# Kernel optimization log

Measured on AMD Instinct MI355X. Metric: run time of the kernel, lower is better.

## Reference

```python
import jax, jax.numpy as jnp
import numpy as np

B = 8
INPUT_SHAPE = (32, 32, 32)
N = int(np.prod(INPUT_SHAPE))  # 32768
K = 128


def setup_inputs() -> dict:
    key = jax.random.key(0)
    k1, k2, k3, k4 = jax.random.split(key, 4)
    data = jax.random.normal(k1, (B,) + INPUT_SHAPE, dtype=jnp.float32)
    mask = jax.random.uniform(k2, (B,) + INPUT_SHAPE, dtype=jnp.float32)
    mult = jax.random.normal(k3, (N, K), dtype=jnp.float32) * 0.05  # RandomNormal init
    sigma_sq = jax.random.normal(k4, (1,), dtype=jnp.float32) * 0.05
    return {"data": data, "mask": mask, "mult": mult, "sigma_sq": sigma_sq}


def reference(data, mask, mult, sigma_sq):
    # Two-arg branch of SpatiallySparseDense_old.call (a_fact == 1).
    b = data.shape[0]
    n, k = mult.shape
    data_flat = data.reshape(b, n)          # [B, N]
    mask_flat = mask.reshape(b, n)          # [B, N]
    # W0 = mask_flat * mult, per batch: [B, N, K]
    W0 = mask_flat[:, :, None] * mult[None, :, :]
    # Gram matrix W0^T W0 + sigma^2 * I : [B, K, K]
    gram = jnp.einsum('bnk,bnl->bkl', W0, W0)
    seye = sigma_sq[0] * jnp.eye(k, dtype=data.dtype)
    pre = jnp.linalg.inv(gram + seye[None])  # [B, K, K] (matches tf.linalg.inv)
    # m = W0^T data : [B, K, 1]
    m = jnp.einsum('bnk,bn->bk', W0, data_flat)[..., None]
    res = jnp.matmul(pre, m)                # [B, K, 1]
    return res
```

## Files before the change

### kernel.cpp

```cpp
#include <hip/hip_runtime.h>

#define BATCH 8
#define NN 32768
#define KK 128
#define NCHUNK 32
#define CHUNK 1024
#define NST 16
#define NITER 12

typedef __attribute__((ext_vector_type(8)))  _Float16 half8;
typedef __attribute__((ext_vector_type(4)))  _Float16 half4;
typedef __attribute__((ext_vector_type(16))) float    f32x16;

#define MT_OFF   0ull
#define WH_OFF   (MT_OFF + 8388608ull)
#define DH_OFF   (WH_OFF + 524288ull)
#define GP_OFF   (DH_OFF + 524288ull)
#define MP_OFF   (GP_OFF + 5242880ull)
#define G_OFF    (MP_OFF + 131072ull)

__global__ __launch_bounds__(256) void conv_kernel(
    const float* __restrict__ data, const float* __restrict__ mask,
    unsigned char* __restrict__ ws)
{
    const int gid = blockIdx.x * 256 + threadIdx.x;
    const float4 d4 = ((const float4*)data)[gid];
    const float4 m4 = ((const float4*)mask)[gid];
    half4 w = { (_Float16)m4.x, (_Float16)m4.y, (_Float16)m4.z, (_Float16)m4.w };
    half4 d = { (_Float16)d4.x, (_Float16)d4.y, (_Float16)d4.z, (_Float16)d4.w };
    ((half4*)(ws + WH_OFF))[gid] = w;
    ((half4*)(ws + DH_OFF))[gid] = d;
}

__global__ __launch_bounds__(256) void transpose_kernel(
    const float* __restrict__ mult, unsigned char* __restrict__ ws)
{
    __shared__ _Float16 t[128][136];
    const int tid = threadIdx.x;
    const int n0  = blockIdx.x * 128;
    const float4* m4 = (const float4*)mult;
#pragma unroll
    for (int u = 0; u < 16; ++u) {
        const int c16 = u * 256 + tid;
        const int n  = c16 >> 5;
        const int kq = c16 & 31;
        float4 v = m4[(size_t)(n0 + n) * 32 + kq];
        half4 h = { (_Float16)v.x, (_Float16)v.y, (_Float16)v.z, (_Float16)v.w };
        *(half4*)&t[n][kq * 4] = h;
    }
    __syncthreads();
    _Float16* mt = (_Float16*)(ws + MT_OFF);
    const int k = tid & 127, nh = tid >> 7;
#pragma unroll
    for (int i = 0; i < 8; ++i) {
        const int nb = nh * 64 + i * 8;
        half8 v;
#pragma unroll
        for (int j = 0; j < 8; ++j) v[j] = t[nb + j][k];
        *(half8*)(mt + (size_t)k * NN + n0 + nb) = v;
    }
}

__global__ __launch_bounds__(256, 1) void gram_kernel(
    unsigned char* __restrict__ ws)
{
    __shared__ unsigned char smem[36864];
    const int tid = threadIdx.x;
    const int b     = blockIdx.x >> 5;
    const int chunk = blockIdx.x & 31;
    const int n0    = chunk * CHUNK;
    const int w = tid >> 6, l = tid & 63;

    const _Float16* mt = (const _Float16*)(ws + MT_OFF);

    if (tid < 128) {
        half8 wv = *(const half8*)((const _Float16*)(ws + WH_OFF) + (size_t)b * NN + n0 + tid * 8);
        half8 dv = *(const half8*)((const _Float16*)(ws + DH_OFF) + (size_t)b * NN + n0 + tid * 8);
        *(half8*)(smem + 32768 + tid * 16) = wv;
        *(half8*)(smem + 34816 + tid * 16) = dv;
    }

    const int krow = tid >> 3;
    const int gd   = tid & 7;
    const _Float16* gsrc0 = mt + (size_t)krow * NN + n0 + gd * 8;
    const int wslot = (gd ^ (krow & 7)) * 16;

    uint4 S0, S1, S2, S3;
#define GLOAD(st_) { const _Float16* p = gsrc0 + (size_t)(st_) * 64;          \
        S0 = *(const uint4*)(p);                                              \
        S1 = *(const uint4*)(p + (size_t)32 * NN);                            \
        S2 = *(const uint4*)(p + (size_t)64 * NN);                            \
        S3 = *(const uint4*)(p + (size_t)96 * NN); }
#define DSWRITE(buf_) { unsigned char* bp = smem + (buf_) * 16384 + krow * 128 + wslot; \
        *(uint4*)(bp)         = S0;  *(uint4*)(bp + 4096)  = S1;              \
        *(uint4*)(bp + 8192)  = S2;  *(uint4*)(bp + 12288) = S3; }

    const int frow  = (l & 31) * 128;
    const int fslot = ((w * 2 + (l >> 5)) ^ (l & 7)) * 16;
    const int wdoff = w * 32 + (l >> 5) * 16;

    f32x16 a00 = {}, a01 = {}, a02 = {}, a03 = {}, a11 = {},
           a12 = {}, a13 = {}, a22 = {}, a23 = {}, a33 = {};
    float macc0 = 0.f, macc1 = 0.f, macc2 = 0.f, macc3 = 0.f;

    GLOAD(0);
    __syncthreads();
    DSWRITE(0);
    GLOAD(1);
    __syncthreads();

#pragma unroll 2
    for (int st = 0; st < NST; ++st) {
        const int cur = st & 1;
        if (st < NST - 1) {
            DSWRITE(cur ^ 1);
            if (st < NST - 2) GLOAD(st + 2);
        }
        const unsigned char* tb = smem + cur * 16384;
        const half8 wf = *(const half8*)(smem + 32768 + st * 128 + wdoff);
        const half8 df = *(const half8*)(smem + 34816 + st * 128 + wdoff);
        half8 f0 = *(const half8*)(tb +     0 + frow + fslot) * wf;
        half8 f1 = *(const half8*)(tb +  4096 + frow + fslot) * wf;
        half8 f2 = *(const half8*)(tb +  8192 + frow + fslot) * wf;
        half8 f3 = *(const half8*)(tb + 12288 + frow + fslot) * wf;
#pragma unroll
        for (int j = 0; j < 8; ++j) {
            const float dj = (float)df[j];
            macc0 = fmaf((float)f0[j], dj, macc0);
            macc1 = fmaf((float)f1[j], dj, macc1);
            macc2 = fmaf((float)f2[j], dj, macc2);
            macc3 = fmaf((float)f3[j], dj, macc3);
        }
        a00 = __builtin_amdgcn_mfma_f32_32x32x16_f16(f0, f0, a00, 0, 0, 0);
        a01 = __builtin_amdgcn_mfma_f32_32x32x16_f16(f0, f1, a01, 0, 0, 0);
        a02 = __builtin_amdgcn_mfma_f32_32x32x16_f16(f0, f2, a02, 0, 0, 0);
        a03 = __builtin_amdgcn_mfma_f32_32x32x16_f16(f0, f3, a03, 0, 0, 0);
        a11 = __builtin_amdgcn_mfma_f32_32x32x16_f16(f1, f1, a11, 0, 0, 0);
        a12 = __builtin_amdgcn_mfma_f32_32x32x16_f16(f1, f2, a12, 0, 0, 0);
        a13 = __builtin_amdgcn_mfma_f32_32x32x16_f16(f1, f3, a13, 0, 0, 0);
        a22 = __builtin_amdgcn_mfma_f32_32x32x16_f16(f2, f2, a22, 0, 0, 0);
        a23 = __builtin_amdgcn_mfma_f32_32x32x16_f16(f2, f3, a23, 0, 0, 0);
        a33 = __builtin_amdgcn_mfma_f32_32x32x16_f16(f3, f3, a33, 0, 0, 0);
        __syncthreads();
    }

    {
        float* M = (float*)(smem + 32768);
        const int base = (w * 2 + (l >> 5)) * 128 + (l & 31);
        M[base +  0] = macc0;  M[base + 32] = macc1;
        M[base + 64] = macc2;  M[base + 96] = macc3;
    }
    _Float16* Gp = (_Float16*)(ws + GP_OFF) + (size_t)(b * NCHUNK + chunk) * 10240;
    float* Mp = (float*)(ws + MP_OFF) + (size_t)(b * NCHUNK + chunk) * KK;
    float* R = (float*)smem;

#define PHASE(p_, A0_, A1_)                                                    \
    {                                                                          \
        *(f32x16*)(R + (w * 2 + 0) * 1024 + l * 16) = A0_;                     \
        *(f32x16*)(R + (w * 2 + 1) * 1024 + l * 16) = A1_;                     \
        __syncthreads();                                                       \
        _Pragma("unroll")                                                      \
        for (int pass = 0; pass < 2; ++pass) {                                 \
            const int e = pass * 1024 + tid * 4;                               \
            float4 s0 = *(float4*)(R + e);                                     \
            float4 s1 = *(float4*)(R + 2048 + e);                              \
            float4 s2 = *(float4*)(R + 4096 + e);                              \
            float4 s3 = *(float4*)(R + 6144 + e);                              \
            float sx = s0.x + s1.x + s2.x + s3.x;                              \
            float sy = s0.y + s1.y + s2.y + s3.y;                              \
            float sz = s0.z + s1.z + s2.z + s3.z;                              \
            float sw = s0.w + s1.w + s2.w + s3.w;                              \
            half4 h = { (_Float16)sx, (_Float16)sy, (_Float16)sz, (_Float16)sw }; \
            *(half4*)(Gp + (p_) * 2048 + e) = h;                               \
        }                                                                      \
        if ((p_) == 0 && tid < 128) {                                          \
            const float* M = (const float*)(smem + 32768);                     \
            float s = 0.f;                                                     \
            _Pragma("unroll")                                                  \
            for (int c8 = 0; c8 < 8; ++c8) s += M[c8 * 128 + tid];             \
            Mp[tid] = s;                                                       \
        }                                                                      \
        __syncthreads();                                                       \
    }

    PHASE(0, a00, a01)
    PHASE(1, a02, a03)
    PHASE(2, a11, a12)
    PHASE(3, a13, a22)
    PHASE(4, a23, a33)
#undef PHASE
#undef GLOAD
#undef DSWRITE
}

__global__ __launch_bounds__(256) void reduce_kernel(
    const float* __restrict__ sig, unsigned char* __restrict__ ws)
{
    const int tid = threadIdx.x;
    const int b  = blockIdx.x >> 6;
    const int jb = blockIdx.x & 63;
    const int j  = jb * 256 + tid;
    const int r = j >> 7, c = j & 127;
    const int t = r >> 5, u = c >> 5;
    int tt, uu, rr, cc;
    if (t <= u) { tt = t; uu = u; rr = r & 31; cc = c & 31; }
    else        { tt = u; uu = t; rr = c & 31; cc = r & 31; }
    const int tidx = tt * 4 - tt * (tt + 1) / 2 + uu;
    const int lane = cc + 32 * ((rr >> 2) & 1);
    const int reg  = (rr & 3) + 4 * ((rr >> 3) & 3);
    const _Float16* Gp = (const _Float16*)(ws + GP_OFF)
                       + (size_t)b * NCHUNK * 10240
                       + (size_t)tidx * 1024 + lane * 16 + reg;
    float s = 0.f;
#pragma unroll
    for (int ch = 0; ch < NCHUNK; ++ch) s += (float)Gp[(size_t)ch * 10240];
    if (r == c) s += sig[0];
    ((float*)(ws + G_OFF))[(size_t)b * 16384 + j] = s;
}

__device__ __forceinline__ float blockDot(float a, float bvl, float* red)
{
    float v = a * bvl;
#pragma unroll
    for (int off = 32; off > 0; off >>= 1) v += __shfl_down(v, off, 64);
    const int wid = threadIdx.x >> 6;
    if ((threadIdx.x & 63) == 0) red[wid] = v;
    __syncthreads();
    float s = red[0] + red[1];
    __syncthreads();
    return s;
}

__global__ __launch_bounds__(128, 1) void solve_kernel(
    const unsigned char* __restrict__ ws, float* __restrict__ out)
{
    const int b = blockIdx.x;
    const int i = threadIdx.x;

    __shared__ float ps[KK];
    __shared__ float red[2];

    const float* G  = (const float*)(ws + G_OFF) + (size_t)b * 16384;
    const float* Mp = (const float*)(ws + MP_OFF) + (size_t)b * NCHUNK * KK;

    float Gr[KK];
#pragma unroll
    for (int j = 0; j < KK; ++j) Gr[j] = G[j * KK + i];

    float mvv = 0.f;
#pragma unroll
    for (int ch = 0; ch < NCHUNK; ++ch) mvv += Mp[ch * KK + i];

    float x = 0.f, r = mvv, p = r;
    ps[i] = p;
    float rs = blockDot(r, r, red);

    for (int it = 0; it < NITER; ++it) {
        float q0 = 0.f, q1 = 0.f, q2 = 0.f, q3 = 0.f;
#pragma unroll
        for (int u = 0; u < 32; ++u) {
            float4 pv = *reinterpret_cast<const float4*>(&ps[4 * u]);
            q0 = fmaf(Gr[4 * u + 0], pv.x, q0);
            q1 = fmaf(Gr[4 * u + 1], pv.y, q1);
            q2 = fmaf(Gr[4 * u + 2], pv.z, q2);
            q3 = fmaf(Gr[4 * u + 3], pv.w, q3);
        }
        float q = (q0 + q1) + (q2 + q3);

        float pq    = blockDot(p, q, red);
        float alpha = rs / (pq + 1e-30f);
        x = fmaf(alpha, p, x);
        r = fmaf(-alpha, q, r);
        float rs2  = blockDot(r, r, red);
        float beta = rs2 / (rs + 1e-30f);
        rs = rs2;
        p  = fmaf(beta, p, r);
        ps[i] = p;
        __syncthreads();
    }
    out[(size_t)b * KK + i] = x;
}

extern "C" void kernel_launch(void* const* d_in, const int* in_sizes, int n_in,
                              void* d_out, int out_size, void* d_ws, size_t ws_size,
                              hipStream_t stream)
{
    const float* data = (const float*)d_in[0];
    const float* mask = (const float*)d_in[1];
    const float* mult = (const float*)d_in[2];
    const float* sig  = (const float*)d_in[3];
    unsigned char* ws = (unsigned char*)d_ws;
    float* out = (float*)d_out;

    conv_kernel     <<<256, 256, 0, stream>>>(data, mask, ws);
    transpose_kernel<<<256, 256, 0, stream>>>(mult, ws);
    gram_kernel     <<<BATCH * NCHUNK, 256, 0, stream>>>(ws);
    reduce_kernel   <<<BATCH * 64, 256, 0, stream>>>(sig, ws);
    solve_kernel    <<<BATCH, 128, 0, stream>>>(ws, out);
}
```

Baseline: 117.7 us.

## Fuse conversion into transpose, swizzle LDS, vectorize reduce, cut solver iterations

```diff
diff --git a/kernel.cpp b/kernel.cpp
--- a/kernel.cpp
+++ b/kernel.cpp
@@ -6,7 +6,7 @@
 #define NCHUNK 32
 #define CHUNK 1024
 #define NST 16
-#define NITER 12
+#define NITER 8
 
 typedef __attribute__((ext_vector_type(8)))  _Float16 half8;
 typedef __attribute__((ext_vector_type(4)))  _Float16 half4;
@@ -19,45 +19,53 @@
 #define MP_OFF   (GP_OFF + 5242880ull)
 #define G_OFF    (MP_OFF + 131072ull)
 
-__global__ __launch_bounds__(256) void conv_kernel(
+__global__ __launch_bounds__(256) void prep_kernel(
     const float* __restrict__ data, const float* __restrict__ mask,
-    unsigned char* __restrict__ ws)
-{
-    const int gid = blockIdx.x * 256 + threadIdx.x;
-    const float4 d4 = ((const float4*)data)[gid];
-    const float4 m4 = ((const float4*)mask)[gid];
-    half4 w = { (_Float16)m4.x, (_Float16)m4.y, (_Float16)m4.z, (_Float16)m4.w };
-    half4 d = { (_Float16)d4.x, (_Float16)d4.y, (_Float16)d4.z, (_Float16)d4.w };
-    ((half4*)(ws + WH_OFF))[gid] = w;
-    ((half4*)(ws + DH_OFF))[gid] = d;
-}
-
-__global__ __launch_bounds__(256) void transpose_kernel(
     const float* __restrict__ mult, unsigned char* __restrict__ ws)
 {
     __shared__ _Float16 t[128][136];
     const int tid = threadIdx.x;
     const int n0  = blockIdx.x * 128;
-    const float4* m4 = (const float4*)mult;
+
+    {
+        const int b = tid >> 5, q = tid & 31;
+        const size_t src = (size_t)b * NN + n0 + q * 4;
+        const float4 d4 = *(const float4*)(data + src);
+        const float4 m4 = *(const float4*)(mask + src);
+        half4 w = { (_Float16)m4.x, (_Float16)m4.y, (_Float16)m4.z, (_Float16)m4.w };
+        half4 d = { (_Float16)d4.x, (_Float16)d4.y, (_Float16)d4.z, (_Float16)d4.w };
+        *(half4*)((_Float16*)(ws + WH_OFF) + src) = w;
+        *(half4*)((_Float16*)(ws + DH_OFF) + src) = d;
+    }
+
+    const float4* m4p = (const float4*)mult;
 #pragma unroll
     for (int u = 0; u < 16; ++u) {
         const int c16 = u * 256 + tid;
         const int n  = c16 >> 5;
         const int kq = c16 & 31;
-        float4 v = m4[(size_t)(n0 + n) * 32 + kq];
+        float4 v = m4p[(size_t)(n0 + n) * 32 + kq];
         half4 h = { (_Float16)v.x, (_Float16)v.y, (_Float16)v.z, (_Float16)v.w };
-        *(half4*)&t[n][kq * 4] = h;
-    }
-    __syncthreads();
+        const int c4s = kq ^ ((n >> 3) & 7);
+        *(half4*)&t[n][c4s * 4] = h;
+    }
+    __syncthreads();
+
     _Float16* mt = (_Float16*)(ws + MT_OFF);
-    const int k = tid & 127, nh = tid >> 7;
+    const int g = tid & 15;
 #pragma unroll
     for (int i = 0; i < 8; ++i) {
-        const int nb = nh * 64 + i * 8;
+        const int k = (tid >> 4) + i * 16;
+        const int c4 = (k >> 2) ^ 7;
         half8 v;
 #pragma unroll
-        for (int j = 0; j < 8; ++j) v[j] = t[nb + j][k];
-        *(half8*)(mt + (size_t)k * NN + n0 + nb) = v;
+        for (int j = 0; j < 8; ++j) {
+            const int n = g * 8 + j;
+            const int cs = (k >> 2) ^ ((n >> 3) & 7);
+            v[j] = t[n][cs * 4 + (k & 3)];
+        }
+        (void)c4;
+        *(half8*)(mt + (size_t)k * NN + n0 + g * 8) = v;
     }
 }
 
@@ -197,25 +205,40 @@
     const float* __restrict__ sig, unsigned char* __restrict__ ws)
 {
     const int tid = threadIdx.x;
-    const int b  = blockIdx.x >> 6;
-    const int jb = blockIdx.x & 63;
-    const int j  = jb * 256 + tid;
-    const int r = j >> 7, c = j & 127;
-    const int t = r >> 5, u = c >> 5;
-    int tt, uu, rr, cc;
-    if (t <= u) { tt = t; uu = u; rr = r & 31; cc = c & 31; }
-    else        { tt = u; uu = t; rr = c & 31; cc = r & 31; }
-    const int tidx = tt * 4 - tt * (tt + 1) / 2 + uu;
-    const int lane = cc + 32 * ((rr >> 2) & 1);
-    const int reg  = (rr & 3) + 4 * ((rr >> 3) & 3);
+    const int b  = blockIdx.x / 5;
+    const int t2 = blockIdx.x % 5;
+
+    const int e_local = tid * 8;
+    const int tile = t2 * 2 + (e_local >> 10);
+    const int off  = e_local & 1023;
+    const int lane = off >> 4;
+    const int r0   = off & 15;
+
     const _Float16* Gp = (const _Float16*)(ws + GP_OFF)
-                       + (size_t)b * NCHUNK * 10240
-                       + (size_t)tidx * 1024 + lane * 16 + reg;
-    float s = 0.f;
-#pragma unroll
-    for (int ch = 0; ch < NCHUNK; ++ch) s += (float)Gp[(size_t)ch * 10240];
-    if (r == c) s += sig[0];
-    ((float*)(ws + G_OFF))[(size_t)b * 16384 + j] = s;
+                       + (size_t)b * NCHUNK * 10240 + (size_t)t2 * 2048 + e_local;
+    float s[8] = {0.f,0.f,0.f,0.f,0.f,0.f,0.f,0.f};
+#pragma unroll
+    for (int ch = 0; ch < NCHUNK; ++ch) {
+        half8 v = *(const half8*)(Gp + (size_t)ch * 10240);
+#pragma unroll
+        for (int j = 0; j < 8; ++j) s[j] += (float)v[j];
+    }
+
+    static const int TT[10] = {0,0,0,0,1,1,1,2,2,3};
+    static const int UU[10] = {0,1,2,3,1,2,3,2,3,3};
+    const int tt = TT[tile], uu = UU[tile];
+    const int C = uu * 32 + (lane & 31);
+    float* G = (float*)(ws + G_OFF) + (size_t)b * 16384;
+    const float sg = sig[0];
+#pragma unroll
+    for (int j = 0; j < 8; ++j) {
+        const int reg = r0 + j;
+        const int row = (reg & 3) + 8 * (reg >> 2) + 4 * (lane >> 5);
+        const int Rr = tt * 32 + row;
+        float v = s[j];
+        G[Rr * KK + C] = (Rr == C) ? v + sg : v;
+        if (tt != uu) G[C * KK + Rr] = v;
+    }
 }
 
 __device__ __forceinline__ float blockDot(float a, float bvl, float* red)
@@ -292,9 +315,8 @@
     unsigned char* ws = (unsigned char*)d_ws;
     float* out = (float*)d_out;
 
-    conv_kernel     <<<256, 256, 0, stream>>>(data, mask, ws);
-    transpose_kernel<<<256, 256, 0, stream>>>(mult, ws);
-    gram_kernel     <<<BATCH * NCHUNK, 256, 0, stream>>>(ws);
-    reduce_kernel   <<<BATCH * 64, 256, 0, stream>>>(sig, ws);
-    solve_kernel    <<<BATCH, 128, 0, stream>>>(ws, out);
-}
+    prep_kernel  <<<256, 256, 0, stream>>>(data, mask, mult, ws);
+    gram_kernel  <<<BATCH * NCHUNK, 256, 0, stream>>>(ws);
+    reduce_kernel<<<BATCH * 5, 256, 0, stream>>>(sig, ws);
+    solve_kernel <<<BATCH, 128, 0, stream>>>(ws, out);
+}
```

Measured after the change: 103.1 us. 12.4% less time.
